# Kernel optimization log

Hardware: AMD Instinct MI355X
Metric: run time of the kernel (lower is better)

The kernel has to match this reference:

```python
import jax, jax.numpy as jnp
import numpy as np

L, HID, NH, AD, FF = 6, 512, 8, 64, 2048
G, ST, NF, RA, RD = 8, 512, 25, 16, 20
T = G + 4 * ST  # 2056 tokens


def _ln(x, g, b, eps=1e-5):
    m = jnp.mean(x, axis=-1, keepdims=True)
    v = jnp.mean((x - m) ** 2, axis=-1, keepdims=True)
    return (x - m) * jax.lax.rsqrt(v + eps) * g + b


def _expand4(m, g):
    top = jnp.concatenate([m[:, :g, :g], jnp.repeat(m[:, :g, g:], 4, axis=2)], axis=2)
    bot = jnp.concatenate([jnp.repeat(m[:, g:, :g], 4, axis=1),
                           jnp.repeat(jnp.repeat(m[:, g:, g:], 4, axis=1), 4, axis=2)], axis=2)
    return jnp.concatenate([top, bot], axis=1)


def setup_inputs() -> dict:
    key = jax.random.key(0)
    ks = iter(jax.random.split(key, 48))
    n = lambda shape, s=0.02: (jax.random.normal(next(ks), shape, jnp.float32) * s)
    N = G + ST
    inp = {
        "obj_input": jax.random.normal(next(ks), (1, G, NF, 4), jnp.float32),
        "obj_scale": jax.random.normal(next(ks), (1, G, NF, 2), jnp.float32),
        "st_input0": jax.random.normal(next(ks), (1, ST, 10), jnp.float32),
        "rpe_a": jax.random.randint(next(ks), (1, N, N), 0, RA, jnp.int32),
        "rpe_d": jax.random.randint(next(ks), (1, N, N), 0, RD + 1, jnp.int32),
        "mask": jnp.zeros((1, N, N), jnp.float32),
        # projection heads
        "Wpg": n((4 * NF, HID)), "bpg": jnp.zeros((HID,)),
        "pg_g": jnp.ones((HID,)), "pg_b": jnp.zeros((HID,)),
        "Wps": n((2, HID)), "bps": jnp.zeros((HID,)),
        "ps_g": jnp.ones((HID,)), "ps_b": jnp.zeros((HID,)),
        # relative position embeddings
        "emb_a": n((RA, NH)), "emb_d": n((RD + 1, NH)),
        # stacked transformer layer params
        "Wq": n((L, HID, NH * AD)), "bq": jnp.zeros((L, NH * AD)),
        "Wk": n((L, HID, NH * AD)), "bk": jnp.zeros((L, NH * AD)),
        "Wv": n((L, HID, NH * AD)), "bv": jnp.zeros((L, NH * AD)),
        "Wo": n((L, NH * AD, HID)), "bo": jnp.zeros((L, HID)),
        "W1": n((L, HID, FF)), "b1": jnp.zeros((L, FF)),
        "W2": n((L, FF, HID)), "b2": jnp.zeros((L, HID)),
        "ln1_g": jnp.ones((L, HID)), "ln1_b": jnp.zeros((L, HID)),
        "ln2_g": jnp.ones((L, HID)), "ln2_b": jnp.zeros((L, HID)),
    }
    return inp


def reference(obj_input, obj_scale, st_input0, rpe_a, rpe_d, mask,
              Wpg, bpg, pg_g, pg_b, Wps, bps, ps_g, ps_b, emb_a, emb_d,
              Wq, bq, Wk, bk, Wv, bv, Wo, bo, W1, b1, W2, b2,
              ln1_g, ln1_b, ln2_g, ln2_b):
    g = obj_input.shape[1]
    # token embeddings: objects + strokes (4 points of 2 coords each)
    st = st_input0[:, :, :8].reshape(1, -1, 2)                       # [1, 4*ST, 2]
    obj_emb = jax.nn.leaky_relu(_ln(obj_input.reshape(1, g, -1) @ Wpg + bpg, pg_g, pg_b))
    st_emb = jax.nn.leaky_relu(_ln(st @ Wps + bps, ps_g, ps_b))
    x = jnp.concatenate([obj_emb, st_emb], axis=1)                   # [1, T, HID]
    t = x.shape[1]
    # relative-position bias: embed expanded angle/distance indices
    pos = emb_a[_expand4(rpe_a, g)] + emb_d[_expand4(rpe_d, g)]      # [1, T, T, NH]
    pos = jnp.transpose(pos, (0, 3, 1, 2))                           # [1, NH, T, T]
    msk = _expand4(mask, g)[:, None]                                 # [1, 1, T, T]
    inv_sqrt_d = np.float32(1.0 / np.sqrt(AD))
    for l in range(Wq.shape[0]):
        q = (x @ Wq[l] + bq[l]).reshape(1, t, NH, AD)
        k = (x @ Wk[l] + bk[l]).reshape(1, t, NH, AD)
        v = (x @ Wv[l] + bv[l]).reshape(1, t, NH, AD)
        # note: bias added BEFORE scaling, then mask (matches torch source)
        scores = (jnp.einsum('bqhd,bkhd->bhqk', q, k) + pos) * inv_sqrt_d + msk
        att = jax.nn.softmax(scores, axis=-1)
        o = jnp.einsum('bhqk,bkhd->bqhd', att, v).reshape(1, t, NH * AD)
        x = _ln(x + o @ Wo[l] + bo[l], ln1_g[l], ln1_b[l])
        h = jax.nn.leaky_relu(x @ W1[l] + b1[l])
        x = _ln(x + h @ W2[l] + b2[l], ln2_g[l], ln2_b[l])
    return x
```

## Files before the change

kernel.cpp:

```cpp
#include <hip/hip_runtime.h>
#include <math.h>

#define T_TOK 2056
#define TP 2176
#define TK 2112
#define HIDDEN 512
#define NHEAD 8
#define ADIM 64
#define FFDIM 2048
#define NLAYER 6
#define NORIG 520
#define NOBJ 8
#define NSPLIT 4
#define FSPLIT 8

typedef float f32x4 __attribute__((ext_vector_type(4)));
typedef __attribute__((__ext_vector_type__(8))) __bf16 bf16x8;

#if __has_builtin(__builtin_amdgcn_exp2f)
#define EXP2(x) __builtin_amdgcn_exp2f(x)
#else
#define EXP2(x) exp2f(x)
#endif

__device__ __forceinline__ unsigned short f2bf(float f) {
  unsigned int u = __float_as_uint(f);
  u += 0x7FFFu + ((u >> 16) & 1u);
  return (unsigned short)(u >> 16);
}
__device__ __forceinline__ float bf2f(unsigned short u) {
  return __uint_as_float(((unsigned int)u) << 16);
}
__device__ __forceinline__ unsigned pk2bf(float a, float b) {
#if __has_builtin(__builtin_amdgcn_cvt_pk_bf16_f32)
  auto v = __builtin_amdgcn_cvt_pk_bf16_f32(a, b);
  unsigned u;
  __builtin_memcpy(&u, &v, 4);
  return u;
#else
  return (unsigned)f2bf(a) | ((unsigned)f2bf(b) << 16);
#endif
}

__device__ __forceinline__ void gl_lds16(const void* g, void* l) {
  __builtin_amdgcn_global_load_lds(
      (const __attribute__((address_space(1))) void*)g,
      (__attribute__((address_space(3))) void*)l, 16, 0, 0);
}


__device__ inline float blockReduceSum(float v, float* sb) {
#pragma unroll
  for (int off = 32; off > 0; off >>= 1) v += __shfl_down(v, off, 64);
  int wid = threadIdx.x >> 6;
  __syncthreads();
  if ((threadIdx.x & 63) == 0) sb[wid] = v;
  __syncthreads();
  return sb[0] + sb[1] + sb[2] + sb[3];
}


__global__ __launch_bounds__(256) void embed_kernel(
    const float* __restrict__ obj, const float* __restrict__ st0,
    const float* __restrict__ Wpg, const float* __restrict__ bpg,
    const float* __restrict__ pg_g, const float* __restrict__ pg_b,
    const float* __restrict__ Wps, const float* __restrict__ bps,
    const float* __restrict__ ps_g, const float* __restrict__ ps_b,
    float* __restrict__ x, unsigned short* __restrict__ xb)
{
  __shared__ float sb[4];
  int t = blockIdx.x;
  int j0 = threadIdx.x, j1 = threadIdx.x + 256;
  float a0, a1;
  const float *g, *b;
  if (t < NOBJ) {
    a0 = bpg[j0]; a1 = bpg[j1];
    const float* in = obj + t * 100;
    for (int i = 0; i < 100; i++) {
      float w = in[i];
      a0 += w * Wpg[i * HIDDEN + j0];
      a1 += w * Wpg[i * HIDDEN + j1];
    }
    g = pg_g; b = pg_b;
  } else {
    int tt = t - NOBJ, s = tt >> 2, p = tt & 3;
    float c0 = st0[s * 10 + p * 2], c1 = st0[s * 10 + p * 2 + 1];
    a0 = bps[j0] + c0 * Wps[j0] + c1 * Wps[HIDDEN + j0];
    a1 = bps[j1] + c0 * Wps[j1] + c1 * Wps[HIDDEN + j1];
    g = ps_g; b = ps_b;
  }
  float s1 = blockReduceSum(a0 + a1, sb);
  float s2 = blockReduceSum(a0 * a0 + a1 * a1, sb);
  float m = s1 * (1.0f / HIDDEN);
  float var = s2 * (1.0f / HIDDEN) - m * m;
  float inv = rsqrtf(var + 1e-5f);
  float y0 = (a0 - m) * inv * g[j0] + b[j0];
  float y1 = (a1 - m) * inv * g[j1] + b[j1];
  y0 = y0 >= 0.f ? y0 : 0.01f * y0;
  y1 = y1 >= 0.f ? y1 : 0.01f * y1;
  x[t * HIDDEN + j0] = y0;
  x[t * HIDDEN + j1] = y1;
  xb[t * HIDDEN + j0] = f2bf(y0);
  xb[t * HIDDEN + j1] = f2bf(y1);
}

__global__ __launch_bounds__(256) void padzero(unsigned short* __restrict__ xb) {
  int i = blockIdx.x * 256 + threadIdx.x;
  if (i < (TP - T_TOK) * HIDDEN) xb[T_TOK * HIDDEN + i] = 0;
}


__global__ __launch_bounds__(256) void posbuild(
    const int* __restrict__ rpe_a, const int* __restrict__ rpe_d,
    const float* __restrict__ emb_a, const float* __restrict__ emb_d,
    const float* __restrict__ mask, unsigned short* __restrict__ posb)
{
  int i = blockIdx.x;
  for (int j = threadIdx.x; j < NORIG; j += 256) {
    int a = rpe_a[i * NORIG + j];
    int d = rpe_d[i * NORIG + j];
    float mk = mask[i * NORIG + j];
#pragma unroll
    for (int h = 0; h < NHEAD; h++) {
      float v = ((emb_a[a * NHEAD + h] + emb_d[d * NHEAD + h]) * 0.125f + mk) * 1.44269504f;
      posb[(h * NORIG + i) * NORIG + j] = f2bf(v);
    }
  }
}


__global__ __launch_bounds__(256) void wtrans(
    const float* __restrict__ Wq, const float* __restrict__ Wk, const float* __restrict__ Wv,
    const float* __restrict__ Wo, const float* __restrict__ W1, const float* __restrict__ W2,
    unsigned short* __restrict__ Wqkvt, unsigned short* __restrict__ Wot,
    unsigned short* __restrict__ W1t, unsigned short* __restrict__ W2t)
{
  __shared__ float t[64 * 65];
  int b = blockIdx.x;
  const float* src; unsigned short* dst; int N, K, tk, tn;
  if (b < 192) {
    int m = b >> 6, bb = b & 63;
    src = m == 0 ? Wq : m == 1 ? Wk : Wv;
    dst = Wqkvt + m * 512 * 512;
    K = 512; N = 512; tk = bb & 7; tn = bb >> 3;
  } else if (b < 256) {
    int bb = b - 192; src = Wo; dst = Wot; K = 512; N = 512; tk = bb & 7; tn = bb >> 3;
  } else if (b < 512) {
    int bb = b - 256; src = W1; dst = W1t; K = 512; N = 2048; tk = bb & 7; tn = bb >> 3;
  } else {
    int bb = b - 512; src = W2; dst = W2t; K = 2048; N = 512; tk = bb & 31; tn = bb >> 5;
  }
  int k0 = tk * 64, n0 = tn * 64;
  int tid = threadIdx.x;
  int r = tid >> 2, c0 = (tid & 3) * 16;
  const float* sp = src + (k0 + r) * N + n0 + c0;
#pragma unroll
  for (int q = 0; q < 4; q++) {
    float4 f = *(const float4*)(sp + q * 4);
    t[r * 65 + c0 + q * 4 + 0] = f.x;
    t[r * 65 + c0 + q * 4 + 1] = f.y;
    t[r * 65 + c0 + q * 4 + 2] = f.z;
    t[r * 65 + c0 + q * 4 + 3] = f.w;
  }
  __syncthreads();
  unsigned short vals[16];
#pragma unroll
  for (int j = 0; j < 16; j++) vals[j] = f2bf(t[(c0 + j) * 65 + r]);
  unsigned short* dp = dst + (n0 + r) * K + k0 + c0;
  *(int4*)dp = *(int4*)&vals[0];
  *(int4*)(dp + 8) = *(int4*)&vals[8];
}


__global__ __launch_bounds__(256) void gemm_bt(
    const unsigned short* __restrict__ A, int lda,
    const unsigned short* __restrict__ Bt, int ldb, int K, int mode,
    const float* __restrict__ b0, const float* __restrict__ b1, const float* __restrict__ b2,
    unsigned short* __restrict__ d0, unsigned short* __restrict__ d1, unsigned short* __restrict__ d2,
    float* __restrict__ df, int ldc)
{
  __shared__ unsigned short As[2][64 * 32];
  __shared__ unsigned short Bs[2][128 * 32];
  const int tid = threadIdx.x;
  const int lane = tid & 63, wave = tid >> 6;
  const int l15 = lane & 15, quad = lane >> 4;
  const int rowBase = blockIdx.y * 64, colBase = blockIdx.x * 128;
  const int mw = (wave & 1) * 32, nw = (wave >> 1) * 64;
  const int zz = blockIdx.z;
  const int kLen = K / gridDim.z;
  const int kb0 = zz * kLen;
  const int nIter = kLen >> 5;
  const int srow = tid >> 2;
  const int kchunk = (tid & 3) ^ ((srow >> 1) & 3);
  const unsigned short* Ag  = A  + (size_t)(rowBase + srow) * lda + kb0 + kchunk * 8;
  const unsigned short* Bg0 = Bt + (size_t)(colBase + srow) * ldb + kb0 + kchunk * 8;
  const unsigned short* Bg1 = Bg0 + (size_t)64 * ldb;
  int aoff[2], boff[4];
#pragma unroll
  for (int mt = 0; mt < 2; mt++) {
    int row = mw + mt * 16 + l15;
    aoff[mt] = row * 32 + ((quad ^ ((row >> 1) & 3)) * 8);
  }
#pragma unroll
  for (int nt = 0; nt < 4; nt++) {
    int row = nw + nt * 16 + l15;
    boff[nt] = row * 32 + ((quad ^ ((row >> 1) & 3)) * 8);
  }
  f32x4 acc[2][4];
#pragma unroll
  for (int i = 0; i < 2; i++)
#pragma unroll
    for (int j = 0; j < 4; j++) acc[i][j] = (f32x4){0.f, 0.f, 0.f, 0.f};

  gl_lds16(Ag,  (unsigned short*)As[0] + tid * 8);
  gl_lds16(Bg0, (unsigned short*)Bs[0] + tid * 8);
  gl_lds16(Bg1, (unsigned short*)Bs[0] + 2048 + tid * 8);

  for (int it = 0; it < nIter; ++it) {
    const int cur = it & 1, nxt = cur ^ 1;
    __syncthreads();
    if (it + 1 < nIter) {
      int koff = (it + 1) * 32;
      gl_lds16(Ag + koff,  (unsigned short*)As[nxt] + tid * 8);
      gl_lds16(Bg0 + koff, (unsigned short*)Bs[nxt] + tid * 8);
      gl_lds16(Bg1 + koff, (unsigned short*)Bs[nxt] + 2048 + tid * 8);
    }
    bf16x8 af[2], bfr[4];
#pragma unroll
    for (int mt = 0; mt < 2; mt++)
      af[mt] = *(const bf16x8*)&As[cur][aoff[mt]];
#pragma unroll
    for (int nt = 0; nt < 4; nt++)
      bfr[nt] = *(const bf16x8*)&Bs[cur][boff[nt]];
#pragma unroll
    for (int mt = 0; mt < 2; mt++)
#pragma unroll
      for (int nt = 0; nt < 4; nt++)
        acc[mt][nt] = __builtin_amdgcn_mfma_f32_16x16x32_bf16(af[mt], bfr[nt], acc[mt][nt], 0, 0, 0);
  }

  float* dfz = df + (size_t)zz * TP * ldc;
#pragma unroll
  for (int mt = 0; mt < 2; mt++) {
#pragma unroll
    for (int nt = 0; nt < 4; nt++) {
#pragma unroll
      for (int r = 0; r < 4; r++) {
        int row = rowBase + mw + mt * 16 + quad * 4 + r;
        int col = colBase + nw + nt * 16 + l15;
        float v = acc[mt][nt][r];
        if (mode == 0) {
          int seg = col >> 9, cc = col & 511;
          const float* bs = seg == 0 ? b0 : seg == 1 ? b1 : b2;
          unsigned short* dst = seg == 0 ? d0 : seg == 1 ? d1 : d2;
          int hd = cc >> 6, d = cc & 63;
          float t = v + bs[cc];
          if (seg == 0) t *= 0.180336880111f;
          dst[(hd * TP + row) * 64 + d] = f2bf(t);
        } else if (mode == 1) {
          dfz[row * ldc + col] = v;
        } else {
          float t = v + b0[col];
          t = t >= 0.f ? t : 0.01f * t;
          d0[row * ldc + col] = f2bf(t);
        }
      }
    }
  }
}


__global__ __launch_bounds__(256) void vt_trans(
    const unsigned short* __restrict__ vh, unsigned short* __restrict__ vt)
{
  __shared__ unsigned short t[64 * 72];
  int kt = blockIdx.x, h = blockIdx.y;
  int tid = threadIdx.x;
  int r0 = tid >> 3, cs = (tid & 7) * 8;
  const unsigned short* src = vh + (h * TP + kt * 64 + r0) * 64 + cs;
  *(int4*)&t[r0 * 72 + cs] = *(const int4*)src;
  *(int4*)&t[(r0 + 32) * 72 + cs] = *(const int4*)(src + 32 * 64);
  __syncthreads();
  int d = tid >> 2, c0 = (tid & 3) * 16;
  unsigned short vals[16];
#pragma unroll
  for (int j = 0; j < 16; j++) vals[j] = t[(c0 + j) * 72 + d];
  unsigned short* dst = vt + (h * 64 + d) * TK + kt * 64 + c0;
  *(int4*)dst = *(int4*)&vals[0];
  *(int4*)(dst + 8) = *(int4*)&vals[8];
}


__global__ __launch_bounds__(256) void flash_attn(
    const unsigned short* __restrict__ qh, const unsigned short* __restrict__ kh,
    const unsigned short* __restrict__ vt, const unsigned short* __restrict__ posb,
    unsigned short* __restrict__ Opart, float* __restrict__ lbuf)
{
  __shared__ unsigned short Ks[64 * 72];
  __shared__ unsigned short Vs[80 * 88];
  __shared__ unsigned short Ps[64 * 72];
  __shared__ float pt[24 * 24];
  const int tid = threadIdx.x;
  const int lane = tid & 63, wave = tid >> 6;
  const int l15 = lane & 15, quad = lane >> 4;
  const int qt = blockIdx.x, h = blockIdx.y, z = blockIdx.z;
  const int q0 = qt * 64;
  const int qrow = q0 + wave * 16 + l15;
  const unsigned short* qbp = qh + (h * TP + qrow) * 64;
  bf16x8 qf0 = *(const bf16x8*)(qbp + quad * 8);
  bf16x8 qf1 = *(const bf16x8*)(qbp + 32 + quad * 8);
  f32x4 O[5];
#pragma unroll
  for (int nt = 0; nt < 5; nt++) O[nt] = (f32x4){0.f, 0.f, 0.f, 0.f};
  for (int idx = tid; idx < 16 * 88; idx += 256) {
    int rr = idx / 88, cc = idx - rr * 88;
    Vs[(64 + rr) * 88 + cc] = (rr == 0) ? 0x3F80 : 0;
  }
  const int oq0 = q0 < 8 ? q0 : 8 + ((q0 - 8) >> 2);
  const int qe = min(q0 + 63, T_TOK - 1);
  const int nq = (qe < 8 ? qe : 8 + ((qe - 8) >> 2)) - oq0 + 1;
  int myq[4];
#pragma unroll
  for (int r = 0; r < 4; r++) {
    int qr = q0 + wave * 16 + quad * 4 + r;
    myq[r] = (qr < 8 ? qr : 8 + ((qr - 8) >> 2)) - oq0;
  }
  const int sr = tid >> 3, sc = (tid & 7) * 8;
  const unsigned short* kgb = kh + (h * TP + sr) * 64 + sc;
  const unsigned short* vgb = vt + (h * 64 + sr) * TK + sc;
  const int ptrow = tid >> 3, ptc0 = (tid & 7) * 3;
  const bool prok = (ptrow < 24) && (ptrow < nq);

  const int nT = (33 - z + FSPLIT - 1) / FSPLIT;
  int kb = z * 64;
  int4 kv0 = *(const int4*)(kgb + kb * 64);
  int4 kv1 = *(const int4*)(kgb + (kb + 32) * 64);
  int4 vv0 = *(const int4*)(vgb + kb);
  int4 vv1 = *(const int4*)(vgb + 32 * TK + kb);
  float ppf0, ppf1, ppf2;
  {
    int ok0n = kb < 8 ? kb : 8 + ((kb - 8) >> 2);
    int ken = min(kb + 63, T_TOK - 1);
    int nkn = (ken < 8 ? ken : 8 + ((ken - 8) >> 2)) - ok0n + 1;
    const unsigned short* prow = posb + (h * NORIG + oq0 + ptrow) * NORIG + ok0n;
    ppf0 = (prok && ptc0 + 0 < nkn) ? bf2f(prow[ptc0 + 0]) : 0.f;
    ppf1 = (prok && ptc0 + 1 < nkn) ? bf2f(prow[ptc0 + 1]) : 0.f;
    ppf2 = (prok && ptc0 + 2 < nkn) ? bf2f(prow[ptc0 + 2]) : 0.f;
  }

  for (int it = 0; it < nT; ++it) {
    const int kbCur = kb;
    const int ok0c = kbCur < 8 ? kbCur : 8 + ((kbCur - 8) >> 2);
    __syncthreads();
    *(int4*)&Ks[sr * 72 + sc] = kv0;
    *(int4*)&Ks[(sr + 32) * 72 + sc] = kv1;
    *(int4*)&Vs[sr * 88 + sc] = vv0;
    *(int4*)&Vs[(sr + 32) * 88 + sc] = vv1;
    if (ptrow < 24) {
      pt[ptrow * 24 + ptc0 + 0] = ppf0;
      pt[ptrow * 24 + ptc0 + 1] = ppf1;
      pt[ptrow * 24 + ptc0 + 2] = ppf2;
    }
    __syncthreads();
    kb += FSPLIT * 64;
    if (it + 1 < nT) {
      kv0 = *(const int4*)(kgb + kb * 64);
      kv1 = *(const int4*)(kgb + (kb + 32) * 64);
      vv0 = *(const int4*)(vgb + kb);
      vv1 = *(const int4*)(vgb + 32 * TK + kb);
      int ok0n = kb < 8 ? kb : 8 + ((kb - 8) >> 2);
      int ken = min(kb + 63, T_TOK - 1);
      int nkn = (ken < 8 ? ken : 8 + ((ken - 8) >> 2)) - ok0n + 1;
      const unsigned short* prow = posb + (h * NORIG + oq0 + ptrow) * NORIG + ok0n;
      ppf0 = (prok && ptc0 + 0 < nkn) ? bf2f(prow[ptc0 + 0]) : 0.f;
      ppf1 = (prok && ptc0 + 1 < nkn) ? bf2f(prow[ptc0 + 1]) : 0.f;
      ppf2 = (prok && ptc0 + 2 < nkn) ? bf2f(prow[ptc0 + 2]) : 0.f;
    }
    f32x4 S[4];
#pragma unroll
    for (int nt = 0; nt < 4; nt++) S[nt] = (f32x4){0.f, 0.f, 0.f, 0.f};
#pragma unroll
    for (int nt = 0; nt < 4; nt++) {
      bf16x8 kf0 = *(const bf16x8*)&Ks[(nt * 16 + l15) * 72 + quad * 8];
      bf16x8 kf1 = *(const bf16x8*)&Ks[(nt * 16 + l15) * 72 + 32 + quad * 8];
      S[nt] = __builtin_amdgcn_mfma_f32_16x16x32_bf16(qf0, kf0, S[nt], 0, 0, 0);
      S[nt] = __builtin_amdgcn_mfma_f32_16x16x32_bf16(qf1, kf1, S[nt], 0, 0, 0);
    }
    int okp[4]; bool cval[4];
#pragma unroll
    for (int nt = 0; nt < 4; nt++) {
      int c = kbCur + nt * 16 + l15;
      cval[nt] = c < T_TOK;
      okp[nt] = (c < 8 ? c : 8 + ((c - 8) >> 2)) - ok0c;
    }
    const int prb = wave * 16 + quad * 4;
#pragma unroll
    for (int nt = 0; nt < 4; nt++) {
      const int cidx = nt * 16 + l15;
      float a0 = cval[nt] ? fminf(S[nt][0] + pt[myq[0] * 24 + okp[nt]], 86.f) : -1e30f;
      float a1 = cval[nt] ? fminf(S[nt][1] + pt[myq[1] * 24 + okp[nt]], 86.f) : -1e30f;
      float a2 = cval[nt] ? fminf(S[nt][2] + pt[myq[2] * 24 + okp[nt]], 86.f) : -1e30f;
      float a3 = cval[nt] ? fminf(S[nt][3] + pt[myq[3] * 24 + okp[nt]], 86.f) : -1e30f;
      unsigned u01 = pk2bf(EXP2(a0), EXP2(a1));
      unsigned u23 = pk2bf(EXP2(a2), EXP2(a3));
      Ps[(prb + 0) * 72 + cidx] = (unsigned short)u01;
      Ps[(prb + 1) * 72 + cidx] = (unsigned short)(u01 >> 16);
      Ps[(prb + 2) * 72 + cidx] = (unsigned short)u23;
      Ps[(prb + 3) * 72 + cidx] = (unsigned short)(u23 >> 16);
    }
    bf16x8 pa0 = *(const bf16x8*)&Ps[(wave * 16 + l15) * 72 + quad * 8];
    bf16x8 pa1 = *(const bf16x8*)&Ps[(wave * 16 + l15) * 72 + 32 + quad * 8];
#pragma unroll
    for (int nt = 0; nt < 5; nt++) {
      bf16x8 vb0 = *(const bf16x8*)&Vs[(nt * 16 + l15) * 88 + quad * 8];
      bf16x8 vb1 = *(const bf16x8*)&Vs[(nt * 16 + l15) * 88 + 32 + quad * 8];
      O[nt] = __builtin_amdgcn_mfma_f32_16x16x32_bf16(pa0, vb0, O[nt], 0, 0, 0);
      O[nt] = __builtin_amdgcn_mfma_f32_16x16x32_bf16(pa1, vb1, O[nt], 0, 0, 0);
    }
  }
#pragma unroll
  for (int r = 0; r < 4; r++) {
    int orow = q0 + wave * 16 + quad * 4 + r;
    size_t base = ((size_t)(z * NHEAD + h) * TK + orow);
    if (l15 == 0) lbuf[base] = O[4][r];
#pragma unroll
    for (int nt = 0; nt < 4; nt++)
      Opart[base * 64 + nt * 16 + l15] = f2bf(O[nt][r]);
  }
}


__global__ __launch_bounds__(256) void flash_merge(
    const unsigned short* __restrict__ Opart, const float* __restrict__ lbuf,
    unsigned short* __restrict__ ob)
{
  int idx = blockIdx.x * 256 + threadIdx.x;
  if (idx >= T_TOK * HIDDEN) return;
  int row = idx >> 9, c = idx & 511;
  int h = c >> 6, d = c & 63;
  float num = 0.f, den = 0.f;
#pragma unroll
  for (int s = 0; s < FSPLIT; s++) {
    size_t base = ((size_t)(s * NHEAD + h) * TK + row);
    den += lbuf[base];
    num += bf2f(Opart[base * 64 + d]);
  }
  ob[idx] = f2bf(num / den);
}


__global__ __launch_bounds__(256) void ln_residual4(
    float* __restrict__ x, const float* __restrict__ parts,
    const float* __restrict__ bias,
    const float* __restrict__ g, const float* __restrict__ b,
    unsigned short* __restrict__ xb)
{
  __shared__ float sb[4];
  int row = blockIdx.x;
  int j0 = threadIdx.x, j1 = threadIdx.x + 256;
  int base = row * HIDDEN;
  const size_t ss = (size_t)TP * HIDDEN;
  float v0 = x[base + j0] + bias[j0] + parts[base + j0] + parts[ss + base + j0]
           + parts[2 * ss + base + j0] + parts[3 * ss + base + j0];
  float v1 = x[base + j1] + bias[j1] + parts[base + j1] + parts[ss + base + j1]
           + parts[2 * ss + base + j1] + parts[3 * ss + base + j1];
  float s1 = blockReduceSum(v0 + v1, sb);
  float s2 = blockReduceSum(v0 * v0 + v1 * v1, sb);
  float m = s1 * (1.0f / HIDDEN);
  float var = s2 * (1.0f / HIDDEN) - m * m;
  float inv = rsqrtf(var + 1e-5f);
  float y0 = (v0 - m) * inv * g[j0] + b[j0];
  float y1 = (v1 - m) * inv * g[j1] + b[j1];
  x[base + j0] = y0;
  x[base + j1] = y1;
  xb[base + j0] = f2bf(y0);
  xb[base + j1] = f2bf(y1);
}

__global__ __launch_bounds__(256) void copy_out(
    const float4* __restrict__ src, float4* __restrict__ dst, int n4)
{
  int i = blockIdx.x * 256 + threadIdx.x;
  if (i < n4) dst[i] = src[i];
}


extern "C" void kernel_launch(void* const* d_in, const int* in_sizes, int n_in,
                              void* d_out, int out_size, void* d_ws, size_t ws_size,
                              hipStream_t stream) {
  const float* obj   = (const float*)d_in[0];
  const float* st0   = (const float*)d_in[2];
  const int*   rpe_a = (const int*)d_in[3];
  const int*   rpe_d = (const int*)d_in[4];
  const float* mask  = (const float*)d_in[5];
  const float* Wpg = (const float*)d_in[6];  const float* bpg = (const float*)d_in[7];
  const float* pg_g = (const float*)d_in[8]; const float* pg_b = (const float*)d_in[9];
  const float* Wps = (const float*)d_in[10]; const float* bps = (const float*)d_in[11];
  const float* ps_g = (const float*)d_in[12];const float* ps_b = (const float*)d_in[13];
  const float* emb_a = (const float*)d_in[14];
  const float* emb_d = (const float*)d_in[15];
  const float* Wq = (const float*)d_in[16]; const float* bq = (const float*)d_in[17];
  const float* Wk = (const float*)d_in[18]; const float* bk = (const float*)d_in[19];
  const float* Wv = (const float*)d_in[20]; const float* bv = (const float*)d_in[21];
  const float* Wo = (const float*)d_in[22]; const float* bo = (const float*)d_in[23];
  const float* W1 = (const float*)d_in[24]; const float* b1 = (const float*)d_in[25];
  const float* W2 = (const float*)d_in[26]; const float* b2 = (const float*)d_in[27];
  const float* ln1_g = (const float*)d_in[28]; const float* ln1_b = (const float*)d_in[29];
  const float* ln2_g = (const float*)d_in[30]; const float* ln2_b = (const float*)d_in[31];

  char* p = (char*)d_ws;
  auto alloc = [&](size_t bytes) { char* q = p; p += (bytes + 255) & ~(size_t)255; return q; };
  float*          x      = (float*)alloc((size_t)T_TOK * HIDDEN * 4);
  unsigned short* xb     = (unsigned short*)alloc((size_t)TP * HIDDEN * 2);
  char*           u1     = (char*)alloc((size_t)TP * FFDIM * 2);
  unsigned short* qhb    = (unsigned short*)u1;
  unsigned short* khb    = qhb + (size_t)NHEAD * TP * ADIM;
  unsigned short* vhb    = khb + (size_t)NHEAD * TP * ADIM;
  unsigned short* vtb    = vhb + (size_t)NHEAD * TP * ADIM;
  unsigned short* hb     = (unsigned short*)u1;
  unsigned short* ob     = (unsigned short*)alloc((size_t)TP * HIDDEN * 2);
  size_t opartB = (size_t)FSPLIT * NHEAD * TK * ADIM * 2;
  size_t partsB = (size_t)NSPLIT * TP * HIDDEN * 4;
  size_t u2B = opartB + (size_t)FSPLIT * NHEAD * TK * 4;
  if (partsB > u2B) u2B = partsB;
  char*           u2     = (char*)alloc(u2B);
  unsigned short* Opart  = (unsigned short*)u2;
  float*          lbb    = (float*)(u2 + opartB);
  float*          parts  = (float*)u2;
  unsigned short* posb   = (unsigned short*)alloc((size_t)NHEAD * NORIG * NORIG * 2);
  size_t perLayerW = ((size_t)1536 * 512 + 512 * 512 + 2048 * 512 + 512 * 2048) * 2;
  size_t baseUsed = (size_t)(p - (char*)d_ws);
  bool hoist = (baseUsed + 6 * perLayerW + 2048) <= ws_size;
  int nWsets = hoist ? 6 : 1;
  unsigned short* Wsets = (unsigned short*)alloc(perLayerW * nWsets);
  if ((size_t)(p - (char*)d_ws) > ws_size) return;

  auto wq_t = [&](int l) { return Wsets + (hoist ? l : 0) * (perLayerW / 2); };
  auto wo_t = [&](int l) { return wq_t(l) + (size_t)1536 * 512; };
  auto w1_t = [&](int l) { return wo_t(l) + (size_t)512 * 512; };
  auto w2_t = [&](int l) { return w1_t(l) + (size_t)2048 * 512; };

  float* out = (float*)d_out;

  embed_kernel<<<T_TOK, 256, 0, stream>>>(obj, st0, Wpg, bpg, pg_g, pg_b,
                                          Wps, bps, ps_g, ps_b, x, xb);
  padzero<<<((TP - T_TOK) * HIDDEN + 255) / 256, 256, 0, stream>>>(xb);
  posbuild<<<NORIG, 256, 0, stream>>>(rpe_a, rpe_d, emb_a, emb_d, mask, posb);
  if (hoist) {
    for (int l = 0; l < NLAYER; l++)
      wtrans<<<768, 256, 0, stream>>>(
          Wq + l * 512 * 512, Wk + l * 512 * 512, Wv + l * 512 * 512,
          Wo + l * 512 * 512, W1 + l * 512 * 2048, W2 + l * 2048 * 512,
          wq_t(l), wo_t(l), w1_t(l), w2_t(l));
  }

  for (int l = 0; l < NLAYER; l++) {
    if (!hoist) {
      wtrans<<<768, 256, 0, stream>>>(
          Wq + l * 512 * 512, Wk + l * 512 * 512, Wv + l * 512 * 512,
          Wo + l * 512 * 512, W1 + l * 512 * 2048, W2 + l * 2048 * 512,
          wq_t(l), wo_t(l), w1_t(l), w2_t(l));
    }
    gemm_bt<<<dim3(12, 34, 1), 256, 0, stream>>>(
        xb, HIDDEN, wq_t(l), HIDDEN, HIDDEN, 0,
        bq + l * 512, bk + l * 512, bv + l * 512, qhb, khb, vhb, nullptr, 0);
    vt_trans<<<dim3(33, 8), 256, 0, stream>>>(vhb, vtb);
    flash_attn<<<dim3(33, 8, FSPLIT), 256, 0, stream>>>(
        qhb, khb, vtb, posb, Opart, lbb);
    flash_merge<<<(T_TOK * HIDDEN + 255) / 256, 256, 0, stream>>>(Opart, lbb, ob);
    gemm_bt<<<dim3(4, 34, NSPLIT), 256, 0, stream>>>(
        ob, HIDDEN, wo_t(l), HIDDEN, HIDDEN, 1,
        nullptr, nullptr, nullptr, nullptr, nullptr, nullptr, parts, HIDDEN);
    ln_residual4<<<T_TOK, 256, 0, stream>>>(x, parts, bo + l * 512,
                                            ln1_g + l * 512, ln1_b + l * 512, xb);
    gemm_bt<<<dim3(16, 34, 1), 256, 0, stream>>>(
        xb, HIDDEN, w1_t(l), HIDDEN, HIDDEN, 2,
        b1 + l * 2048, nullptr, nullptr, hb, nullptr, nullptr, nullptr, FFDIM);
    gemm_bt<<<dim3(4, 34, NSPLIT), 256, 0, stream>>>(
        hb, FFDIM, w2_t(l), FFDIM, FFDIM, 1,
        nullptr, nullptr, nullptr, nullptr, nullptr, nullptr, parts, HIDDEN);
    ln_residual4<<<T_TOK, 256, 0, stream>>>(x, parts, b2 + l * 512,
                                            ln2_g + l * 512, ln2_b + l * 512, xb);
  }

  int n4 = T_TOK * HIDDEN / 4;
  copy_out<<<(n4 + 255) / 256, 256, 0, stream>>>((const float4*)x, (float4*)out, n4);
}
```

Baseline: 957.8 us.

## Double GEMM K-tile, write V transposed from QKV GEMM, fold pad-zeroing into embed

The bf16 GEMM now stages 64-wide K tiles instead of 32 and uses an 8-way XOR swizzle, which halves the number of loop iterations and barriers. The QKV GEMM epilogue writes V directly in transposed [head,d,token] layout, so the separate vt_trans kernel and its intermediate buffer are gone. Zeroing of the padding rows moves into the embed kernel through extra blocks, which removes the padzero launch. The cost is double the LDS per block, which may lower occupancy, plus scattered strided stores for V in the epilogue.

```diff
diff --git a/kernel.cpp b/kernel.cpp
--- a/kernel.cpp
+++ b/kernel.cpp
@@ -71,6 +71,11 @@
   __shared__ float sb[4];
   int t = blockIdx.x;
   int j0 = threadIdx.x, j1 = threadIdx.x + 256;
+  if (t >= T_TOK) {
+    xb[t * HIDDEN + j0] = 0;
+    xb[t * HIDDEN + j1] = 0;
+    return;
+  }
   float a0, a1;
   const float *g, *b;
   if (t < NOBJ) {
@@ -102,11 +107,6 @@
   x[t * HIDDEN + j1] = y1;
   xb[t * HIDDEN + j0] = f2bf(y0);
   xb[t * HIDDEN + j1] = f2bf(y1);
-}
-
-__global__ __launch_bounds__(256) void padzero(unsigned short* __restrict__ xb) {
-  int i = blockIdx.x * 256 + threadIdx.x;
-  if (i < (TP - T_TOK) * HIDDEN) xb[T_TOK * HIDDEN + i] = 0;
 }
 
 
@@ -179,8 +179,8 @@
     unsigned short* __restrict__ d0, unsigned short* __restrict__ d1, unsigned short* __restrict__ d2,
     float* __restrict__ df, int ldc)
 {
-  __shared__ unsigned short As[2][64 * 32];
-  __shared__ unsigned short Bs[2][128 * 32];
+  __shared__ unsigned short As[2][64 * 64];
+  __shared__ unsigned short Bs[2][128 * 64];
   const int tid = threadIdx.x;
   const int lane = tid & 63, wave = tid >> 6;
   const int l15 = lane & 15, quad = lane >> 4;
@@ -189,22 +189,32 @@
   const int zz = blockIdx.z;
   const int kLen = K / gridDim.z;
   const int kb0 = zz * kLen;
-  const int nIter = kLen >> 5;
-  const int srow = tid >> 2;
-  const int kchunk = (tid & 3) ^ ((srow >> 1) & 3);
-  const unsigned short* Ag  = A  + (size_t)(rowBase + srow) * lda + kb0 + kchunk * 8;
-  const unsigned short* Bg0 = Bt + (size_t)(colBase + srow) * ldb + kb0 + kchunk * 8;
-  const unsigned short* Bg1 = Bg0 + (size_t)64 * ldb;
-  int aoff[2], boff[4];
+  const int nIter = kLen >> 6;
+  const int as0 = tid, as1 = tid + 256;
+  const int ar0 = as0 >> 3, ar1 = as1 >> 3;
+  const unsigned short* Ag0 = A + (size_t)(rowBase + ar0) * lda + kb0 + (((as0 & 7) ^ (ar0 & 7)) * 8);
+  const unsigned short* Ag1 = A + (size_t)(rowBase + ar1) * lda + kb0 + (((as1 & 7) ^ (ar1 & 7)) * 8);
+  const unsigned short* Bg[4];
+#pragma unroll
+  for (int j = 0; j < 4; j++) {
+    int s = tid + 256 * j;
+    int r = s >> 3;
+    Bg[j] = Bt + (size_t)(colBase + r) * ldb + kb0 + (((s & 7) ^ (r & 7)) * 8);
+  }
+  int aoff[2][2], boff[4][2];
 #pragma unroll
   for (int mt = 0; mt < 2; mt++) {
     int row = mw + mt * 16 + l15;
-    aoff[mt] = row * 32 + ((quad ^ ((row >> 1) & 3)) * 8);
+#pragma unroll
+    for (int kh = 0; kh < 2; kh++)
+      aoff[mt][kh] = row * 64 + (((quad + kh * 4) ^ (row & 7)) * 8);
   }
 #pragma unroll
   for (int nt = 0; nt < 4; nt++) {
     int row = nw + nt * 16 + l15;
-    boff[nt] = row * 32 + ((quad ^ ((row >> 1) & 3)) * 8);
+#pragma unroll
+    for (int kh = 0; kh < 2; kh++)
+      boff[nt][kh] = row * 64 + (((quad + kh * 4) ^ (row & 7)) * 8);
   }
   f32x4 acc[2][4];
 #pragma unroll
@@ -212,31 +222,38 @@
 #pragma unroll
     for (int j = 0; j < 4; j++) acc[i][j] = (f32x4){0.f, 0.f, 0.f, 0.f};
 
-  gl_lds16(Ag,  (unsigned short*)As[0] + tid * 8);
-  gl_lds16(Bg0, (unsigned short*)Bs[0] + tid * 8);
-  gl_lds16(Bg1, (unsigned short*)Bs[0] + 2048 + tid * 8);
+  gl_lds16(Ag0, (unsigned short*)As[0] + as0 * 8);
+  gl_lds16(Ag1, (unsigned short*)As[0] + as1 * 8);
+#pragma unroll
+  for (int j = 0; j < 4; j++)
+    gl_lds16(Bg[j], (unsigned short*)Bs[0] + (tid + 256 * j) * 8);
 
   for (int it = 0; it < nIter; ++it) {
     const int cur = it & 1, nxt = cur ^ 1;
     __syncthreads();
     if (it + 1 < nIter) {
-      int koff = (it + 1) * 32;
-      gl_lds16(Ag + koff,  (unsigned short*)As[nxt] + tid * 8);
-      gl_lds16(Bg0 + koff, (unsigned short*)Bs[nxt] + tid * 8);
-      gl_lds16(Bg1 + koff, (unsigned short*)Bs[nxt] + 2048 + tid * 8);
-    }
-    bf16x8 af[2], bfr[4];
-#pragma unroll
-    for (int mt = 0; mt < 2; mt++)
-      af[mt] = *(const bf16x8*)&As[cur][aoff[mt]];
-#pragma unroll
-    for (int nt = 0; nt < 4; nt++)
-      bfr[nt] = *(const bf16x8*)&Bs[cur][boff[nt]];
-#pragma unroll
-    for (int mt = 0; mt < 2; mt++)
+      int koff = (it + 1) * 64;
+      gl_lds16(Ag0 + koff, (unsigned short*)As[nxt] + as0 * 8);
+      gl_lds16(Ag1 + koff, (unsigned short*)As[nxt] + as1 * 8);
+#pragma unroll
+      for (int j = 0; j < 4; j++)
+        gl_lds16(Bg[j] + koff, (unsigned short*)Bs[nxt] + (tid + 256 * j) * 8);
+    }
+#pragma unroll
+    for (int kh = 0; kh < 2; kh++) {
+      bf16x8 af[2], bfr[4];
+#pragma unroll
+      for (int mt = 0; mt < 2; mt++)
+        af[mt] = *(const bf16x8*)&As[cur][aoff[mt][kh]];
 #pragma unroll
       for (int nt = 0; nt < 4; nt++)
-        acc[mt][nt] = __builtin_amdgcn_mfma_f32_16x16x32_bf16(af[mt], bfr[nt], acc[mt][nt], 0, 0, 0);
+        bfr[nt] = *(const bf16x8*)&Bs[cur][boff[nt][kh]];
+#pragma unroll
+      for (int mt = 0; mt < 2; mt++)
+#pragma unroll
+        for (int nt = 0; nt < 4; nt++)
+          acc[mt][nt] = __builtin_amdgcn_mfma_f32_16x16x32_bf16(af[mt], bfr[nt], acc[mt][nt], 0, 0, 0);
+    }
   }
 
   float* dfz = df + (size_t)zz * TP * ldc;
@@ -252,11 +269,16 @@
         if (mode == 0) {
           int seg = col >> 9, cc = col & 511;
           const float* bs = seg == 0 ? b0 : seg == 1 ? b1 : b2;
-          unsigned short* dst = seg == 0 ? d0 : seg == 1 ? d1 : d2;
           int hd = cc >> 6, d = cc & 63;
           float t = v + bs[cc];
-          if (seg == 0) t *= 0.180336880111f;
-          dst[(hd * TP + row) * 64 + d] = f2bf(t);
+          if (seg == 0) {
+            t *= 0.180336880111f;
+            d0[(hd * TP + row) * 64 + d] = f2bf(t);
+          } else if (seg == 1) {
+            d1[(hd * TP + row) * 64 + d] = f2bf(t);
+          } else {
+            if (row < TK) d2[(hd * 64 + d) * TK + row] = f2bf(t);
+          }
         } else if (mode == 1) {
           dfz[row * ldc + col] = v;
         } else {
@@ -267,27 +289,6 @@
       }
     }
   }
-}
-
-
-__global__ __launch_bounds__(256) void vt_trans(
-    const unsigned short* __restrict__ vh, unsigned short* __restrict__ vt)
-{
-  __shared__ unsigned short t[64 * 72];
-  int kt = blockIdx.x, h = blockIdx.y;
-  int tid = threadIdx.x;
-  int r0 = tid >> 3, cs = (tid & 7) * 8;
-  const unsigned short* src = vh + (h * TP + kt * 64 + r0) * 64 + cs;
-  *(int4*)&t[r0 * 72 + cs] = *(const int4*)src;
-  *(int4*)&t[(r0 + 32) * 72 + cs] = *(const int4*)(src + 32 * 64);
-  __syncthreads();
-  int d = tid >> 2, c0 = (tid & 3) * 16;
-  unsigned short vals[16];
-#pragma unroll
-  for (int j = 0; j < 16; j++) vals[j] = t[(c0 + j) * 72 + d];
-  unsigned short* dst = vt + (h * 64 + d) * TK + kt * 64 + c0;
-  *(int4*)dst = *(int4*)&vals[0];
-  *(int4*)(dst + 8) = *(int4*)&vals[8];
 }
 
 
@@ -515,8 +516,7 @@
   char*           u1     = (char*)alloc((size_t)TP * FFDIM * 2);
   unsigned short* qhb    = (unsigned short*)u1;
   unsigned short* khb    = qhb + (size_t)NHEAD * TP * ADIM;
-  unsigned short* vhb    = khb + (size_t)NHEAD * TP * ADIM;
-  unsigned short* vtb    = vhb + (size_t)NHEAD * TP * ADIM;
+  unsigned short* vtb    = khb + (size_t)NHEAD * TP * ADIM;
   unsigned short* hb     = (unsigned short*)u1;
   unsigned short* ob     = (unsigned short*)alloc((size_t)TP * HIDDEN * 2);
   size_t opartB = (size_t)FSPLIT * NHEAD * TK * ADIM * 2;
@@ -542,9 +542,8 @@
 
   float* out = (float*)d_out;
 
-  embed_kernel<<<T_TOK, 256, 0, stream>>>(obj, st0, Wpg, bpg, pg_g, pg_b,
-                                          Wps, bps, ps_g, ps_b, x, xb);
-  padzero<<<((TP - T_TOK) * HIDDEN + 255) / 256, 256, 0, stream>>>(xb);
+  embed_kernel<<<TP, 256, 0, stream>>>(obj, st0, Wpg, bpg, pg_g, pg_b,
+                                       Wps, bps, ps_g, ps_b, x, xb);
   posbuild<<<NORIG, 256, 0, stream>>>(rpe_a, rpe_d, emb_a, emb_d, mask, posb);
   if (hoist) {
     for (int l = 0; l < NLAYER; l++)
@@ -563,8 +562,7 @@
     }
     gemm_bt<<<dim3(12, 34, 1), 256, 0, stream>>>(
         xb, HIDDEN, wq_t(l), HIDDEN, HIDDEN, 0,
-        bq + l * 512, bk + l * 512, bv + l * 512, qhb, khb, vhb, nullptr, 0);
-    vt_trans<<<dim3(33, 8), 256, 0, stream>>>(vhb, vtb);
+        bq + l * 512, bk + l * 512, bv + l * 512, qhb, khb, vtb, nullptr, 0);
     flash_attn<<<dim3(33, 8, FSPLIT), 256, 0, stream>>>(
         qhb, khb, vtb, posb, Opart, lbb);
     flash_merge<<<(T_TOK * HIDDEN + 255) / 256, 256, 0, stream>>>(Opart, lbb, ob);
```

New measurement: 937.3 us. -2.1%, faster.
